# Optimization experiments

Measured on AMD Instinct MI355X. Metric: run time of the kernel, lower is better.

Reference implementation:

```python
import jax, jax.numpy as jnp
import numpy as np

EMBED_DIM = 512
NUM_HEADS = 8
HEAD_DIM = EMBED_DIM // NUM_HEADS
PAIR_DIM = 64
B, L = 2, 1024


def setup_inputs() -> dict:
    key = jax.random.key(0)
    ks = jax.random.split(key, 6)
    seq_repr = jax.random.normal(ks[0], (B, L, EMBED_DIM), dtype=jnp.float32)
    pair_repr = jax.random.normal(ks[1], (B, L, L, PAIR_DIM), dtype=jnp.float32)
    # Parameters (stored as [in, out] for x @ W)
    sc = 0.02
    W_qkv = jax.random.normal(ks[2], (EMBED_DIM, 3 * EMBED_DIM), dtype=jnp.float32) * sc
    W_bias = jax.random.normal(ks[3], (PAIR_DIM, NUM_HEADS), dtype=jnp.float32) * sc
    W_out = jax.random.normal(ks[4], (EMBED_DIM, EMBED_DIM), dtype=jnp.float32) * sc
    b_out = jax.random.normal(ks[5], (EMBED_DIM,), dtype=jnp.float32) * sc
    return {"seq_repr": seq_repr, "pair_repr": pair_repr,
            "W_qkv": W_qkv, "W_bias": W_bias, "W_out": W_out, "b_out": b_out}


def reference(seq_repr, pair_repr, W_qkv, W_bias, W_out, b_out):
    b, l, _ = seq_repr.shape
    # pair bias: [B, L, L, pair_dim] -> [B, H, L, L]
    pair_bias = jnp.einsum('bijp,ph->bhij', pair_repr, W_bias)
    qkv = seq_repr @ W_qkv                      # [B, L, 3*E]
    q, k, v = jnp.split(qkv, 3, axis=-1)
    def heads(x):
        return x.reshape(b, l, NUM_HEADS, HEAD_DIM).transpose(0, 2, 1, 3)  # [B,H,L,D]
    q, k, v = heads(q), heads(k), heads(v)
    scale = 1.0 / jnp.sqrt(jnp.asarray(HEAD_DIM, dtype=q.dtype))
    scores = jnp.einsum('bhid,bhjd->bhij', q, k) * scale + pair_bias
    attn = jax.nn.softmax(scores, axis=-1)
    ctx = jnp.einsum('bhij,bhjd->bhid', attn, v)             # [B,H,L,D]
    ctx = ctx.transpose(0, 2, 1, 3).reshape(b, l, EMBED_DIM)
    return ctx @ W_out + b_out
```

## Files before the change

### kernel.cpp

```cpp
#include <hip/hip_runtime.h>
#include <hip/hip_bf16.h>


typedef __attribute__((ext_vector_type(8))) short bf16x8;
typedef __attribute__((ext_vector_type(4))) float f32x4;

__device__ __forceinline__ unsigned pk2(float a, float b) {
    __hip_bfloat16 ha = __float2bfloat16(a);
    __hip_bfloat16 hb = __float2bfloat16(b);
    return (unsigned)__bfloat16_as_ushort(ha) | ((unsigned)__bfloat16_as_ushort(hb) << 16);
}

__device__ __forceinline__ void gl16_nt(const void* g, void* l) {
    __builtin_amdgcn_global_load_lds((const __attribute__((address_space(1))) void*)g,
                                     (__attribute__((address_space(3))) void*)l, 16, 0, 2);
}

__global__ __launch_bounds__(256, 2) void gemm_qkv_kernel(
    const float* __restrict__ A, const float* __restrict__ W,
    unsigned short* __restrict__ qbus, unsigned short* __restrict__ kbus,
    unsigned short* __restrict__ vtbus)
{
    __shared__ float smem[64 * 68];
    float* As = smem;
    float* Bs = smem + 32 * 68;

    const int t  = threadIdx.x;
    const int m0 = blockIdx.y * 64;
    const int n0 = blockIdx.x * 64;
    const int tx = t & 15, ty = t >> 4;

    const int am = t >> 2, ak = (t & 3) * 8;
    const int bk = t >> 3, bn = (t & 7) * 8;

    float acc[4][4] = {};

    for (int k0 = 0; k0 < 512; k0 += 32) {
        float4 a0 = *(const float4*)&A[(size_t)(m0 + am) * 512 + k0 + ak];
        float4 a1 = *(const float4*)&A[(size_t)(m0 + am) * 512 + k0 + ak + 4];
        float4 b0 = *(const float4*)&W[(size_t)(k0 + bk) * 1536 + n0 + bn];
        float4 b1 = *(const float4*)&W[(size_t)(k0 + bk) * 1536 + n0 + bn + 4];
        __syncthreads();
        As[(ak + 0) * 68 + am] = a0.x;
        As[(ak + 1) * 68 + am] = a0.y;
        As[(ak + 2) * 68 + am] = a0.z;
        As[(ak + 3) * 68 + am] = a0.w;
        As[(ak + 4) * 68 + am] = a1.x;
        As[(ak + 5) * 68 + am] = a1.y;
        As[(ak + 6) * 68 + am] = a1.z;
        As[(ak + 7) * 68 + am] = a1.w;
        *(float4*)&Bs[bk * 68 + bn]     = b0;
        *(float4*)&Bs[bk * 68 + bn + 4] = b1;
        __syncthreads();
#pragma unroll
        for (int kk = 0; kk < 32; kk++) {
            float4 a4 = *(float4*)&As[kk * 68 + ty * 4];
            float4 b4 = *(float4*)&Bs[kk * 68 + tx * 4];
            float av[4] = {a4.x, a4.y, a4.z, a4.w};
            float bv[4] = {b4.x, b4.y, b4.z, b4.w};
#pragma unroll
            for (int r = 0; r < 4; r++)
#pragma unroll
                for (int c = 0; c < 4; c++) acc[r][c] += av[r] * bv[c];
        }
    }

    const int sect = n0 >> 9;
    const int h    = (n0 >> 6) & 7;
    const int b    = m0 >> 10;
    const int i0   = m0 & 1023;

    if (sect == 2) {
        __syncthreads();
        float* T = smem;
#pragma unroll
        for (int r = 0; r < 4; r++)
#pragma unroll
            for (int c = 0; c < 4; c++)
                T[(tx * 4 + c) * 68 + (ty * 4 + r)] = acc[r][c];
        __syncthreads();
        const int dp = t >> 2, iq = (t & 3) * 16;
        unsigned short* dst = vtbus + (((size_t)(b * 8 + h)) * 64 + dp) * 1024 + i0 + iq;
#pragma unroll
        for (int u = 0; u < 4; u++) {
            float4 f = *(float4*)&T[dp * 68 + iq + u * 4];
            uint2 pkd; pkd.x = pk2(f.x, f.y); pkd.y = pk2(f.z, f.w);
            *(uint2*)&dst[u * 4] = pkd;
        }
    } else {
        unsigned short* dst = (sect == 0) ? qbus : kbus;
        const float sc = (sect == 0) ? 0.125f : 1.0f;
#pragma unroll
        for (int r = 0; r < 4; r++) {
            const int i = i0 + ty * 4 + r;
#pragma unroll
            for (int c = 0; c < 4; c += 2) {
                unsigned u = pk2(acc[r][c] * sc, acc[r][c + 1] * sc);
                *(unsigned*)&dst[(((size_t)(b * 8 + h)) * 1024 + i) * 64 + tx * 4 + c] = u;
            }
        }
    }
}

__device__ __forceinline__ bf16x8 slab_frag(const char* rowb, int ks, int q4, int sw) {
    const int s0 = ks * 8 + q4 * 2;
    const float4 fa = *(const float4*)(rowb + (((s0    ) ^ sw) << 4));
    const float4 fb = *(const float4*)(rowb + (((s0 + 1) ^ sw) << 4));
    uint4 u;
    u.x = pk2(fa.x, fa.y); u.y = pk2(fa.z, fa.w);
    u.z = pk2(fb.x, fb.y); u.w = pk2(fb.z, fb.w);
    return *(bf16x8*)&u;
}

__global__ __launch_bounds__(512, 2) void attn_kernel(
    const float* __restrict__ pair, const float* __restrict__ Wb,
    const unsigned short* __restrict__ qbus, const unsigned short* __restrict__ kbus,
    const unsigned short* __restrict__ vtbus, float* __restrict__ ctx)
{
    __shared__ __align__(16) char plds[2][65536];
    __shared__ __align__(16) float bias_lds[8 * 16 * 33];
    __shared__ __align__(16) unsigned short pbuf[8 * 16 * 40];

    const int t    = threadIdx.x;
    const int lane = t & 63;
    const int w    = t >> 6;
    const int q4   = lane >> 4;
    const int l15  = lane & 15;

    const int bx   = blockIdx.x;
    const int vbid = (bx & 7) * 32 + (bx >> 3);
    const int b    = vbid >> 7;
    const int i0   = (vbid & 127) * 8;

    for (int z = t; z < 8 * 16 * 33; z += 512) bias_lds[z] = 0.f;

    uint4 wbf[2];
#pragma unroll
    for (int ks = 0; ks < 2; ks++) {
        float f[8];
#pragma unroll
        for (int e = 0; e < 8; e++)
            f[e] = (l15 < 8) ? Wb[(ks * 32 + q4 * 8 + e) * 8 + l15] : 0.f;
        wbf[ks].x = pk2(f[0], f[1]); wbf[ks].y = pk2(f[2], f[3]);
        wbf[ks].z = pk2(f[4], f[5]); wbf[ks].w = pk2(f[6], f[7]);
    }

    uint4 qf[2] = {};
    if (l15 < 8) {
        const unsigned short* qrow = qbus + (size_t)((b * 8 + w) * 1024 + i0 + l15) * 64;
#pragma unroll
        for (int ks = 0; ks < 2; ks++)
            qf[ks] = *(const uint4*)(qrow + ks * 32 + q4 * 8);
    }

    const int rowbase = w * 4 + q4;
    const char* pairB = (const char*)pair + (size_t)(b * 1024 + i0) * 262144
                      + rowbase * 256 + ((l15 ^ (rowbase & 15)) << 4);
    char* ldsW = (char*)plds + w * 1024;

#define STAGE(bufsel, jtn) do {                                         \
        const char* gg = pairB + (size_t)(jtn) * 8192;                  \
        char* ld = ldsW + (bufsel) * 65536;                             \
        _Pragma("unroll")                                               \
        for (int r = 0; r < 8; r++)                                     \
            gl16_nt(gg + r * 262144, ld + r * 8192);                    \
    } while (0)

    STAGE(0, 0);

    f32x4 acc[4];
#pragma unroll
    for (int dn = 0; dn < 4; dn++) acc[dn] = (f32x4){0.f, 0.f, 0.f, 0.f};
    float mrun[4], lrun[4];
#pragma unroll
    for (int rr = 0; rr < 4; rr++) { mrun[rr] = -3.0e38f; lrun[rr] = 0.f; }

    const unsigned short* kbase = kbus + (size_t)((b * 8 + w) * 1024) * 64;
    const unsigned short* vbase = vtbus + (size_t)((b * 8 + w) * 64) * 1024;

    for (int jt = 0; jt < 32; jt++) {
        asm volatile("s_waitcnt vmcnt(0) lgkmcnt(0)" ::: "memory");
        __builtin_amdgcn_sched_barrier(0);
        __builtin_amdgcn_s_barrier();
        __builtin_amdgcn_sched_barrier(0);

        const char* cur = (const char*)plds + (jt & 1) * 65536;

        uint4 kf[2][2], vf[4];
        {
            const unsigned short* kt = kbase + (size_t)(jt * 32) * 64;
#pragma unroll
            for (int jn = 0; jn < 2; jn++)
#pragma unroll
                for (int ks = 0; ks < 2; ks++)
                    kf[jn][ks] = *(const uint4*)(kt + (jn * 16 + l15) * 64 + ks * 32 + q4 * 8);
#pragma unroll
            for (int dn = 0; dn < 4; dn++)
                vf[dn] = *(const uint4*)(vbase + (size_t)(dn * 16 + l15) * 1024 + jt * 32 + q4 * 8);
        }

        if (jt < 31) STAGE((jt + 1) & 1, jt + 1);

        {
            const char* rb0 = cur + (32 * w + l15) * 256;
            const char* rb1 = cur + (32 * w + 16 + l15) * 256;
            f32x4 b0 = {0.f, 0.f, 0.f, 0.f}, b1 = {0.f, 0.f, 0.f, 0.f};
#pragma unroll
            for (int ks = 0; ks < 2; ks++) {
                bf16x8 a0 = slab_frag(rb0, ks, q4, l15);
                b0 = __builtin_amdgcn_mfma_f32_16x16x32_bf16(a0, *(bf16x8*)&wbf[ks], b0, 0, 0, 0);
                bf16x8 a1 = slab_frag(rb1, ks, q4, l15);
                b1 = __builtin_amdgcn_mfma_f32_16x16x32_bf16(a1, *(bf16x8*)&wbf[ks], b1, 0, 0, 0);
            }
            if (l15 < 8) {
                float* bl = &bias_lds[l15 * 528 + w * 33];
#pragma unroll
                for (int rr = 0; rr < 4; rr++) {
                    bl[q4 * 4 + rr]      = b0[rr];
                    bl[16 + q4 * 4 + rr] = b1[rr];
                }
            }
        }

        asm volatile("s_waitcnt lgkmcnt(0)" ::: "memory");
        __builtin_amdgcn_sched_barrier(0);
        __builtin_amdgcn_s_barrier();
        __builtin_amdgcn_sched_barrier(0);

        f32x4 s0, s1;
#pragma unroll
        for (int rr = 0; rr < 4; rr++) {
            s0[rr] = bias_lds[w * 528 + (q4 * 4 + rr) * 33 + l15];
            s1[rr] = bias_lds[w * 528 + (q4 * 4 + rr) * 33 + 16 + l15];
        }
        s0 = __builtin_amdgcn_mfma_f32_16x16x32_bf16(*(bf16x8*)&qf[0], *(bf16x8*)&kf[0][0], s0, 0, 0, 0);
        s0 = __builtin_amdgcn_mfma_f32_16x16x32_bf16(*(bf16x8*)&qf[1], *(bf16x8*)&kf[0][1], s0, 0, 0, 0);
        s1 = __builtin_amdgcn_mfma_f32_16x16x32_bf16(*(bf16x8*)&qf[0], *(bf16x8*)&kf[1][0], s1, 0, 0, 0);
        s1 = __builtin_amdgcn_mfma_f32_16x16x32_bf16(*(bf16x8*)&qf[1], *(bf16x8*)&kf[1][1], s1, 0, 0, 0);

#pragma unroll
        for (int rr = 0; rr < 4; rr++) {
            float x = fmaxf(s0[rr], s1[rr]);
            x = fmaxf(x, __shfl_xor(x, 1));
            x = fmaxf(x, __shfl_xor(x, 2));
            x = fmaxf(x, __shfl_xor(x, 4));
            x = fmaxf(x, __shfl_xor(x, 8));
            const float mnew = fmaxf(mrun[rr], x);
            const float corr = __expf(mrun[rr] - mnew);
            mrun[rr] = mnew;
            const float p0 = __expf(s0[rr] - mnew);
            const float p1 = __expf(s1[rr] - mnew);
            float ts = p0 + p1;
            ts += __shfl_xor(ts, 1);
            ts += __shfl_xor(ts, 2);
            ts += __shfl_xor(ts, 4);
            ts += __shfl_xor(ts, 8);
            lrun[rr] = lrun[rr] * corr + ts;
#pragma unroll
            for (int dn = 0; dn < 4; dn++) acc[dn][rr] *= corr;
            unsigned short* pb = &pbuf[w * 640 + (q4 * 4 + rr) * 40];
            pb[l15]      = __bfloat16_as_ushort(__float2bfloat16(p0));
            pb[16 + l15] = __bfloat16_as_ushort(__float2bfloat16(p1));
        }

        asm volatile("s_waitcnt lgkmcnt(0)" ::: "memory");
        __builtin_amdgcn_sched_barrier(0);

        bf16x8 pfrag = *(bf16x8*)&pbuf[w * 640 + l15 * 40 + q4 * 8];
#pragma unroll
        for (int dn = 0; dn < 4; dn++)
            acc[dn] = __builtin_amdgcn_mfma_f32_16x16x32_bf16(pfrag, *(bf16x8*)&vf[dn], acc[dn], 0, 0, 0);
    }

    if (q4 < 2) {
#pragma unroll
        for (int rr = 0; rr < 4; rr++) {
            const int i = q4 * 4 + rr;
            const float inv = 1.0f / lrun[rr];
            float* crow = ctx + ((size_t)(b * 1024) + i0 + i) * 512 + w * 64;
#pragma unroll
            for (int dn = 0; dn < 4; dn++)
                crow[dn * 16 + l15] = acc[dn][rr] * inv;
        }
    }
#undef STAGE
}

__global__ __launch_bounds__(256, 2) void gemm_out_kernel(
    const float* __restrict__ A, const float* __restrict__ W,
    const float* __restrict__ bias, float* __restrict__ out)
{
    __shared__ float smem[64 * 68];
    float* As = smem;
    float* Bs = smem + 32 * 68;

    const int t  = threadIdx.x;
    const int m0 = blockIdx.y * 64;
    const int n0 = blockIdx.x * 64;
    const int tx = t & 15, ty = t >> 4;

    const int am = t >> 2, ak = (t & 3) * 8;
    const int bk = t >> 3, bn = (t & 7) * 8;

    float acc[4][4] = {};

    for (int k0 = 0; k0 < 512; k0 += 32) {
        float4 a0 = *(const float4*)&A[(size_t)(m0 + am) * 512 + k0 + ak];
        float4 a1 = *(const float4*)&A[(size_t)(m0 + am) * 512 + k0 + ak + 4];
        float4 b0 = *(const float4*)&W[(size_t)(k0 + bk) * 512 + n0 + bn];
        float4 b1 = *(const float4*)&W[(size_t)(k0 + bk) * 512 + n0 + bn + 4];
        __syncthreads();
        As[(ak + 0) * 68 + am] = a0.x;
        As[(ak + 1) * 68 + am] = a0.y;
        As[(ak + 2) * 68 + am] = a0.z;
        As[(ak + 3) * 68 + am] = a0.w;
        As[(ak + 4) * 68 + am] = a1.x;
        As[(ak + 5) * 68 + am] = a1.y;
        As[(ak + 6) * 68 + am] = a1.z;
        As[(ak + 7) * 68 + am] = a1.w;
        *(float4*)&Bs[bk * 68 + bn]     = b0;
        *(float4*)&Bs[bk * 68 + bn + 4] = b1;
        __syncthreads();
#pragma unroll
        for (int kk = 0; kk < 32; kk++) {
            float4 a4 = *(float4*)&As[kk * 68 + ty * 4];
            float4 b4 = *(float4*)&Bs[kk * 68 + tx * 4];
            float av[4] = {a4.x, a4.y, a4.z, a4.w};
            float bv[4] = {b4.x, b4.y, b4.z, b4.w};
#pragma unroll
            for (int r = 0; r < 4; r++)
#pragma unroll
                for (int c = 0; c < 4; c++) acc[r][c] += av[r] * bv[c];
        }
    }

    float4 bo = *(const float4*)&bias[n0 + tx * 4];
    float bv[4] = {bo.x, bo.y, bo.z, bo.w};
#pragma unroll
    for (int r = 0; r < 4; r++) {
        const int m = m0 + ty * 4 + r;
#pragma unroll
        for (int c = 0; c < 4; c++)
            out[(size_t)m * 512 + n0 + tx * 4 + c] = acc[r][c] + bv[c];
    }
}

extern "C" void kernel_launch(void* const* d_in, const int* in_sizes, int n_in,
                              void* d_out, int out_size, void* d_ws, size_t ws_size,
                              hipStream_t stream)
{
    const float* seq  = (const float*)d_in[0];
    const float* pair = (const float*)d_in[1];
    const float* Wqkv = (const float*)d_in[2];
    const float* Wb   = (const float*)d_in[3];
    const float* Wout = (const float*)d_in[4];
    const float* bout = (const float*)d_in[5];
    float* out = (float*)d_out;

    unsigned short* qbus  = (unsigned short*)d_ws;
    unsigned short* kbus  = qbus + (1 << 20);
    unsigned short* vtbus = kbus + (1 << 20);
    float*          ctx   = (float*)(vtbus + (1 << 20));

    gemm_qkv_kernel<<<dim3(24, 32), 256, 0, stream>>>(seq, Wqkv, qbus, kbus, vtbus);
    attn_kernel<<<256, 512, 0, stream>>>(pair, Wb, qbus, kbus, vtbus, ctx);
    gemm_out_kernel<<<dim3(8, 32), 256, 0, stream>>>(ctx, Wout, bout, out);
}
```

Measured before the change: 234.3 us.

## Split attention over key halves with separate log-sum-exp merge kernel

Splits the key dimension of the attention kernel into two halves, doubling the grid to 512 blocks. Each block processes 16 keys per tile instead of 32 with half-size LDS buffers, and launch bounds are raised to allow more resident blocks per CU. Unnormalized partial contexts plus running max and sum are written out, and a new merge kernel combines them with softmax rescaling. The aim is more parallelism and occupancy for the bandwidth-bound pair-bias streaming, at the cost of an extra kernel launch, extra partial-context traffic, and half-empty MFMA tiles (q4>=2 lanes zeroed).

```diff
diff --git a/kernel.cpp b/kernel.cpp
--- a/kernel.cpp
+++ b/kernel.cpp
@@ -112,14 +112,15 @@
     return *(bf16x8*)&u;
 }
 
-__global__ __launch_bounds__(512, 2) void attn_kernel(
+__global__ __launch_bounds__(512, 4) void attn_kernel(
     const float* __restrict__ pair, const float* __restrict__ Wb,
     const unsigned short* __restrict__ qbus, const unsigned short* __restrict__ kbus,
-    const unsigned short* __restrict__ vtbus, float* __restrict__ ctx)
-{
-    __shared__ __align__(16) char plds[2][65536];
-    __shared__ __align__(16) float bias_lds[8 * 16 * 33];
-    __shared__ __align__(16) unsigned short pbuf[8 * 16 * 40];
+    const unsigned short* __restrict__ vtbus, float* __restrict__ cp,
+    float* __restrict__ mlm, float* __restrict__ mll)
+{
+    __shared__ __align__(16) char plds[2][32768];
+    __shared__ __align__(16) float bias_lds[128 * 17];
+    __shared__ __align__(16) unsigned short pbuf[8 * 16 * 24];
 
     const int t    = threadIdx.x;
     const int lane = t & 63;
@@ -128,11 +129,11 @@
     const int l15  = lane & 15;
 
     const int bx   = blockIdx.x;
-    const int vbid = (bx & 7) * 32 + (bx >> 3);
-    const int b    = vbid >> 7;
-    const int i0   = (vbid & 127) * 8;
-
-    for (int z = t; z < 8 * 16 * 33; z += 512) bias_lds[z] = 0.f;
+    const int vbid = ((bx & 7) << 6) | (bx >> 3);
+    const int b    = vbid >> 8;
+    const int rem  = vbid & 255;
+    const int jh   = rem >> 7;
+    const int i0   = (rem & 127) * 8;
 
     uint4 wbf[2];
 #pragma unroll
@@ -153,17 +154,18 @@
             qf[ks] = *(const uint4*)(qrow + ks * 32 + q4 * 8);
     }
 
-    const int rowbase = w * 4 + q4;
+    const int rb = w * 4 + q4;
     const char* pairB = (const char*)pair + (size_t)(b * 1024 + i0) * 262144
-                      + rowbase * 256 + ((l15 ^ (rowbase & 15)) << 4);
+                      + (size_t)jh * 131072
+                      + (rb >> 4) * 262144 + (rb & 15) * 256 + ((l15 ^ (rb & 15)) << 4);
     char* ldsW = (char*)plds + w * 1024;
 
 #define STAGE(bufsel, jtn) do {                                         \
-        const char* gg = pairB + (size_t)(jtn) * 8192;                  \
-        char* ld = ldsW + (bufsel) * 65536;                             \
+        const char* gg = pairB + (size_t)(jtn) * 4096;                  \
+        char* ld = ldsW + (bufsel) * 32768;                             \
         _Pragma("unroll")                                               \
-        for (int r = 0; r < 8; r++)                                     \
-            gl16_nt(gg + r * 262144, ld + r * 8192);                    \
+        for (int r = 0; r < 4; r++)                                     \
+            gl16_nt(gg + (size_t)r * 524288, ld + r * 8192);            \
     } while (0)
 
     STAGE(0, 0);
@@ -175,8 +177,8 @@
 #pragma unroll
     for (int rr = 0; rr < 4; rr++) { mrun[rr] = -3.0e38f; lrun[rr] = 0.f; }
 
-    const unsigned short* kbase = kbus + (size_t)((b * 8 + w) * 1024) * 64;
-    const unsigned short* vbase = vtbus + (size_t)((b * 8 + w) * 64) * 1024;
+    const unsigned short* kbase = kbus + (size_t)((b * 8 + w) * 1024 + jh * 512) * 64;
+    const unsigned short* vbase = vtbus + (size_t)((b * 8 + w) * 64) * 1024 + jh * 512;
 
     for (int jt = 0; jt < 32; jt++) {
         asm volatile("s_waitcnt vmcnt(0) lgkmcnt(0)" ::: "memory");
@@ -184,19 +186,18 @@
         __builtin_amdgcn_s_barrier();
         __builtin_amdgcn_sched_barrier(0);
 
-        const char* cur = (const char*)plds + (jt & 1) * 65536;
-
-        uint4 kf[2][2], vf[4];
+        const char* cur = (const char*)plds + (jt & 1) * 32768;
+
+        uint4 kf[2], vf[4];
         {
-            const unsigned short* kt = kbase + (size_t)(jt * 32) * 64;
-#pragma unroll
-            for (int jn = 0; jn < 2; jn++)
-#pragma unroll
-                for (int ks = 0; ks < 2; ks++)
-                    kf[jn][ks] = *(const uint4*)(kt + (jn * 16 + l15) * 64 + ks * 32 + q4 * 8);
+            const unsigned short* kt = kbase + (size_t)(jt * 16 + l15) * 64;
+#pragma unroll
+            for (int ks = 0; ks < 2; ks++)
+                kf[ks] = *(const uint4*)(kt + ks * 32 + q4 * 8);
 #pragma unroll
             for (int dn = 0; dn < 4; dn++)
-                vf[dn] = *(const uint4*)(vbase + (size_t)(dn * 16 + l15) * 1024 + jt * 32 + q4 * 8);
+                vf[dn] = *(const uint4*)(vbase + (size_t)(dn * 16 + l15) * 1024
+                                         + jt * 16 + (q4 & 1) * 8);
         }
 
         if (jt < 31) STAGE((jt + 1) & 1, jt + 1);
@@ -213,11 +214,10 @@
                 b1 = __builtin_amdgcn_mfma_f32_16x16x32_bf16(a1, *(bf16x8*)&wbf[ks], b1, 0, 0, 0);
             }
             if (l15 < 8) {
-                float* bl = &bias_lds[l15 * 528 + w * 33];
 #pragma unroll
                 for (int rr = 0; rr < 4; rr++) {
-                    bl[q4 * 4 + rr]      = b0[rr];
-                    bl[16 + q4 * 4 + rr] = b1[rr];
+                    bias_lds[(32 * w + q4 * 4 + rr) * 17 + l15]      = b0[rr];
+                    bias_lds[(32 * w + 16 + q4 * 4 + rr) * 17 + l15] = b1[rr];
                 }
             }
         }
@@ -227,20 +227,16 @@
         __builtin_amdgcn_s_barrier();
         __builtin_amdgcn_sched_barrier(0);
 
-        f32x4 s0, s1;
+        f32x4 s;
+#pragma unroll
+        for (int rr = 0; rr < 4; rr++)
+            s[rr] = (q4 < 2) ? bias_lds[((q4 * 4 + rr) * 16 + l15) * 17 + w] : 0.f;
+        s = __builtin_amdgcn_mfma_f32_16x16x32_bf16(*(bf16x8*)&qf[0], *(bf16x8*)&kf[0], s, 0, 0, 0);
+        s = __builtin_amdgcn_mfma_f32_16x16x32_bf16(*(bf16x8*)&qf[1], *(bf16x8*)&kf[1], s, 0, 0, 0);
+
 #pragma unroll
         for (int rr = 0; rr < 4; rr++) {
-            s0[rr] = bias_lds[w * 528 + (q4 * 4 + rr) * 33 + l15];
-            s1[rr] = bias_lds[w * 528 + (q4 * 4 + rr) * 33 + 16 + l15];
-        }
-        s0 = __builtin_amdgcn_mfma_f32_16x16x32_bf16(*(bf16x8*)&qf[0], *(bf16x8*)&kf[0][0], s0, 0, 0, 0);
-        s0 = __builtin_amdgcn_mfma_f32_16x16x32_bf16(*(bf16x8*)&qf[1], *(bf16x8*)&kf[0][1], s0, 0, 0, 0);
-        s1 = __builtin_amdgcn_mfma_f32_16x16x32_bf16(*(bf16x8*)&qf[0], *(bf16x8*)&kf[1][0], s1, 0, 0, 0);
-        s1 = __builtin_amdgcn_mfma_f32_16x16x32_bf16(*(bf16x8*)&qf[1], *(bf16x8*)&kf[1][1], s1, 0, 0, 0);
-
-#pragma unroll
-        for (int rr = 0; rr < 4; rr++) {
-            float x = fmaxf(s0[rr], s1[rr]);
+            float x = s[rr];
             x = fmaxf(x, __shfl_xor(x, 1));
             x = fmaxf(x, __shfl_xor(x, 2));
             x = fmaxf(x, __shfl_xor(x, 4));
@@ -248,9 +244,8 @@
             const float mnew = fmaxf(mrun[rr], x);
             const float corr = __expf(mrun[rr] - mnew);
             mrun[rr] = mnew;
-            const float p0 = __expf(s0[rr] - mnew);
-            const float p1 = __expf(s1[rr] - mnew);
-            float ts = p0 + p1;
+            const float p0 = __expf(s[rr] - mnew);
+            float ts = p0;
             ts += __shfl_xor(ts, 1);
             ts += __shfl_xor(ts, 2);
             ts += __shfl_xor(ts, 4);
@@ -258,15 +253,15 @@
             lrun[rr] = lrun[rr] * corr + ts;
 #pragma unroll
             for (int dn = 0; dn < 4; dn++) acc[dn][rr] *= corr;
-            unsigned short* pb = &pbuf[w * 640 + (q4 * 4 + rr) * 40];
-            pb[l15]      = __bfloat16_as_ushort(__float2bfloat16(p0));
-            pb[16 + l15] = __bfloat16_as_ushort(__float2bfloat16(p1));
+            pbuf[(w * 16 + q4 * 4 + rr) * 24 + l15] =
+                __bfloat16_as_ushort(__float2bfloat16(p0));
         }
 
         asm volatile("s_waitcnt lgkmcnt(0)" ::: "memory");
         __builtin_amdgcn_sched_barrier(0);
 
-        bf16x8 pfrag = *(bf16x8*)&pbuf[w * 640 + l15 * 40 + q4 * 8];
+        bf16x8 pfrag = (bf16x8){0, 0, 0, 0, 0, 0, 0, 0};
+        if (q4 < 2) pfrag = *(bf16x8*)&pbuf[(w * 16 + l15) * 24 + q4 * 8];
 #pragma unroll
         for (int dn = 0; dn < 4; dn++)
             acc[dn] = __builtin_amdgcn_mfma_f32_16x16x32_bf16(pfrag, *(bf16x8*)&vf[dn], acc[dn], 0, 0, 0);
@@ -276,14 +271,44 @@
 #pragma unroll
         for (int rr = 0; rr < 4; rr++) {
             const int i = q4 * 4 + rr;
-            const float inv = 1.0f / lrun[rr];
-            float* crow = ctx + ((size_t)(b * 1024) + i0 + i) * 512 + w * 64;
+            float* crow = cp + (size_t)jh * (2048 * 512)
+                        + ((size_t)(b * 1024) + i0 + i) * 512 + w * 64;
 #pragma unroll
             for (int dn = 0; dn < 4; dn++)
-                crow[dn * 16 + l15] = acc[dn][rr] * inv;
+                crow[dn * 16 + l15] = acc[dn][rr];
+            if (l15 == 0) {
+                const int mi = ((jh * 2 + b) * 8 + w) * 1024 + i0 + i;
+                mlm[mi] = mrun[rr];
+                mll[mi] = lrun[rr];
+            }
         }
     }
 #undef STAGE
+}
+
+__global__ __launch_bounds__(256) void merge_kernel(
+    const float* __restrict__ cp, const float* __restrict__ mlm,
+    const float* __restrict__ mll, float* __restrict__ ctx)
+{
+    const int row = blockIdx.x;
+    const int b   = row >> 10, i = row & 1023;
+    const int t   = threadIdx.x;
+    const int h   = t >> 5;
+
+    const int mi0 = ((0 * 2 + b) * 8 + h) * 1024 + i;
+    const int mi1 = ((1 * 2 + b) * 8 + h) * 1024 + i;
+    const float m0 = mlm[mi0], m1 = mlm[mi1];
+    const float l0 = mll[mi0], l1 = mll[mi1];
+    const float M  = fmaxf(m0, m1);
+    const float w0 = __expf(m0 - M), w1 = __expf(m1 - M);
+    const float inv = 1.0f / (l0 * w0 + l1 * w1);
+
+    const float2 c0 = *(const float2*)&cp[(size_t)row * 512 + t * 2];
+    const float2 c1 = *(const float2*)&cp[(size_t)(2048 * 512) + (size_t)row * 512 + t * 2];
+    float2 o;
+    o.x = (c0.x * w0 + c1.x * w1) * inv;
+    o.y = (c0.y * w0 + c1.y * w1) * inv;
+    *(float2*)&ctx[(size_t)row * 512 + t * 2] = o;
 }
 
 __global__ __launch_bounds__(256, 2) void gemm_out_kernel(
@@ -361,8 +386,12 @@
     unsigned short* kbus  = qbus + (1 << 20);
     unsigned short* vtbus = kbus + (1 << 20);
     float*          ctx   = (float*)(vtbus + (1 << 20));
+    float*          cp    = ctx + (1 << 20);
+    float*          mlm   = cp + (2 << 20);
+    float*          mll   = mlm + (1 << 15);
 
     gemm_qkv_kernel<<<dim3(24, 32), 256, 0, stream>>>(seq, Wqkv, qbus, kbus, vtbus);
-    attn_kernel<<<256, 512, 0, stream>>>(pair, Wb, qbus, kbus, vtbus, ctx);
+    attn_kernel<<<512, 512, 0, stream>>>(pair, Wb, qbus, kbus, vtbus, cp, mlm, mll);
+    merge_kernel<<<2048, 256, 0, stream>>>(cp, mlm, mll, ctx);
     gemm_out_kernel<<<dim3(8, 32), 256, 0, stream>>>(ctx, Wout, bout, out);
 }
```

Measured after the change: 236.2 us. About the same (+0.8%).
